# Kernel tuning notes

Hardware: AMD Instinct MI355X
Metric: run time of the kernel (lower is better)

## Reference

```python
import jax, jax.numpy as jnp
import numpy as np

B, S, D, H = 4, 2048, 1024, 16
DK = D // H
SCALE = 1.0 / np.float32(np.sqrt(DK))


def setup_inputs() -> dict:
    key = jax.random.key(0)
    ks = jax.random.split(key, 11)
    w = lambda k: (jax.random.normal(k, (D, D), jnp.float32) * 0.02)
    b = lambda k: (jax.random.normal(k, (D,), jnp.float32) * 0.02)
    return {
        "Q": jax.random.normal(ks[0], (B, S, D), jnp.float32),
        "K": jax.random.normal(ks[1], (B, S, D), jnp.float32),
        "V": jax.random.normal(ks[2], (B, S, D), jnp.float32),
        "Wq": w(ks[3]), "bq": b(ks[4]),
        "Wk": w(ks[5]), "bk": b(ks[6]),
        "Wv": w(ks[7]), "bv": b(ks[8]),
        "Wo": w(ks[9]), "bo": b(ks[10]),
        # causal mask, broadcast over batch and heads: [1,1,S,S]
        "mask": jnp.tril(jnp.ones((1, 1, S, S), dtype=bool)),
    }


def reference(Q, K, V, Wq, bq, Wk, bk, Wv, bv, Wo, bo, mask):
    def proj(x, W, bias):
        # [B,S,D] -> [B,H,S,DK]
        return (x @ W + bias).reshape(B, S, H, DK).transpose(0, 2, 1, 3)

    q = proj(Q, Wq, bq)
    k = proj(K, Wk, bk)
    v = proj(V, Wv, bv)
    scores = jnp.einsum("bhqd,bhkd->bhqk", q, k) * SCALE  # [B,H,S,S]
    scores = jnp.where(mask, scores, jnp.float32(-1e9))
    attn = jax.nn.softmax(scores, axis=-1)
    out = jnp.einsum("bhqk,bhkd->bhqd", attn, v)  # [B,H,S,DK]
    out = out.transpose(0, 2, 1, 3).reshape(B, S, D)
    return out @ Wo + bo
```

## Files before the change

### kernel.cpp

```cpp
#include <hip/hip_runtime.h>
#include <hip/hip_bf16.h>
#include <stdint.h>

#define BB 4
#define SS 2048
#define DD 1024
#define HH 16
#define DKK 64
#define MM (BB * SS)

typedef __hip_bfloat16 bf16;
typedef __attribute__((ext_vector_type(8))) short frag8;
typedef __attribute__((ext_vector_type(4))) float f32x4;

#define GLDS16(g, l)                                                        \
  __builtin_amdgcn_global_load_lds(                                         \
      (const __attribute__((address_space(1))) void*)(g),                   \
      (__attribute__((address_space(3))) void*)(l), 16, 0, 0)

#define MFMA __builtin_amdgcn_mfma_f32_16x16x32_bf16

__device__ __forceinline__ unsigned short f2bu(float f) {
  __hip_bfloat16 h = __float2bfloat16(f);
  return *reinterpret_cast<unsigned short*>(&h);
}

__global__ __launch_bounds__(1024) void wtrans_kernel(
    const float* __restrict__ W, unsigned short* __restrict__ Wt) {
  __shared__ float tile[32][33];
  const int tx = threadIdx.x, ty = threadIdx.y;
  const int n0 = blockIdx.x * 32, k0 = blockIdx.y * 32;
  tile[ty][tx] = W[(size_t)(k0 + ty) * DD + n0 + tx];
  __syncthreads();
  Wt[(size_t)(n0 + ty) * DD + k0 + tx] = f2bu(tile[tx][ty]);
}

template <int A_BF16, int OUT_MODE>
__global__ __launch_bounds__(256) void gemm_kernel(
    const void* __restrict__ Av, const unsigned short* __restrict__ Wt,
    const float* __restrict__ bias, void* __restrict__ outv, float oscale) {
  constexpr int K = DD;
  constexpr int ASTR = A_BF16 ? 32 : 40;
  __shared__ unsigned short Bs[128 * 32];
  __shared__ unsigned short As[128 * ASTR];
  const int tid = threadIdx.x;
  const int wave = tid >> 6, lane = tid & 63, quad = lane >> 4, l15 = lane & 15;
  const int wr = wave >> 1, wc = wave & 1;
  const int m0 = blockIdx.y * 128, n0 = blockIdx.x * 128;

  f32x4 acc[4][4] = {};

  for (int k0 = 0; k0 < K; k0 += 32) {
#pragma unroll
    for (int c = 0; c < 2; ++c) {
      const int row = c * 64 + wave * 16 + (lane >> 2);
      const int col8 = (lane & 3) * 8;
      const unsigned short* g = &Wt[(size_t)(n0 + row) * K + k0 + col8];
      unsigned off = __builtin_amdgcn_readfirstlane(
          (unsigned)(c * 4096 + wave * 1024));
      GLDS16(g, (char*)&Bs[0] + off);
    }
    if (A_BF16) {
      const unsigned short* A = (const unsigned short*)Av;
#pragma unroll
      for (int c = 0; c < 2; ++c) {
        const int row = c * 64 + wave * 16 + (lane >> 2);
        const int col8 = (lane & 3) * 8;
        const unsigned short* g = &A[(size_t)(m0 + row) * K + k0 + col8];
        unsigned off = __builtin_amdgcn_readfirstlane(
            (unsigned)(c * 4096 + wave * 1024));
        GLDS16(g, (char*)&As[0] + off);
      }
    } else {
      const float* A = (const float*)Av;
#pragma unroll
      for (int it = 0; it < 4; ++it) {
        const int row = tid / 8 + it * 32;
        const int col4 = (tid % 8) * 4;
        const float4 v = *(const float4*)&A[(size_t)(m0 + row) * K + k0 + col4];
        ushort4 u;
        u.x = f2bu(v.x); u.y = f2bu(v.y); u.z = f2bu(v.z); u.w = f2bu(v.w);
        *(ushort4*)&As[row * ASTR + col4] = u;
      }
    }
    __syncthreads();

    frag8 af[4], bfr[4];
#pragma unroll
    for (int mi = 0; mi < 4; ++mi)
      af[mi] = *(const frag8*)&As[(wr * 64 + mi * 16 + l15) * ASTR + quad * 8];
#pragma unroll
    for (int ni = 0; ni < 4; ++ni)
      bfr[ni] = *(const frag8*)&Bs[(wc * 64 + ni * 16 + l15) * 32 + quad * 8];
#pragma unroll
    for (int mi = 0; mi < 4; ++mi)
#pragma unroll
      for (int ni = 0; ni < 4; ++ni)
        acc[mi][ni] = MFMA(af[mi], bfr[ni], acc[mi][ni], 0, 0, 0);
    __syncthreads();
  }

#pragma unroll
  for (int mi = 0; mi < 4; ++mi) {
#pragma unroll
    for (int ni = 0; ni < 4; ++ni) {
#pragma unroll
      for (int r = 0; r < 4; ++r) {
        const int grow = m0 + wr * 64 + mi * 16 + quad * 4 + r;
        const int gcol = n0 + wc * 64 + ni * 16 + l15;
        const float val = (acc[mi][ni][r] + bias[gcol]) * oscale;
        if (OUT_MODE == 2) {
          ((float*)outv)[(size_t)grow * DD + gcol] = val;
        } else {
          const int b = grow / SS, s = grow % SS;
          const int h = gcol / DKK, dk = gcol % DKK;
          unsigned short* o = (unsigned short*)outv;
          if (OUT_MODE == 0)
            o[(((size_t)(b * HH + h)) * SS + s) * DKK + dk] = f2bu(val);
          else
            o[(((size_t)(b * HH + h)) * DKK + dk) * SS + s] = f2bu(val);
        }
      }
    }
  }
}

__global__ __launch_bounds__(256) void fattn_kernel(
    const unsigned short* __restrict__ q, const unsigned short* __restrict__ k,
    const unsigned short* __restrict__ vt, unsigned short* __restrict__ ctx) {
  __shared__ unsigned short Ks[2][64 * 64];
  __shared__ unsigned short Vs[2][64 * 64];
  __shared__ unsigned short P_lds[4][16][36];
  const int tid = threadIdx.x;
  const int wave = tid >> 6, lane = tid & 63, quad = lane >> 4, l15 = lane & 15;
  const int bh = blockIdx.x & 63;
  const int tp = blockIdx.x >> 6;
  const size_t qkb = (size_t)bh * SS * DKK;
  const size_t vtb = (size_t)bh * DKK * SS;
  const int b = bh / HH, h = bh % HH;

  frag8 ones;
#pragma unroll
  for (int s = 0; s < 8; ++s) ones[s] = (short)0x3F80;

  auto stage = [&](int buf, int jt) {
#pragma unroll
    for (int c = 0; c < 2; ++c) {
      const int row = wave * 16 + c * 8 + (lane >> 3);
      const int gc = ((lane & 7) ^ (row & 7)) * 8;
      const unsigned short* g = &k[qkb + (size_t)(jt * 64 + row) * DKK + gc];
      unsigned off = __builtin_amdgcn_readfirstlane(
          (unsigned)(buf * 8192 + (wave * 16 + c * 8) * 128));
      GLDS16(g, (char*)&Ks[0][0] + off);
    }
#pragma unroll
    for (int c = 0; c < 2; ++c) {
      const int row = wave * 16 + c * 8 + (lane >> 3);
      const int gc = ((lane & 7) ^ (row & 7)) * 8;
      const unsigned short* g = &vt[vtb + (size_t)row * SS + jt * 64 + gc];
      unsigned off = __builtin_amdgcn_readfirstlane(
          (unsigned)(buf * 8192 + (wave * 16 + c * 8) * 128));
      GLDS16(g, (char*)&Vs[0][0] + off);
    }
  };

  for (int half = 0; half < 2; ++half) {
    const int t = half ? (31 - tp) : tp;
    const int q0 = t * 64 + wave * 16;

    const frag8 aq0 =
        *(const frag8*)&q[qkb + (size_t)(q0 + l15) * DKK + quad * 8];
    const frag8 aq1 =
        *(const frag8*)&q[qkb + (size_t)(q0 + l15) * DKK + 32 + quad * 8];

    f32x4 oacc[4] = {};
    f32x4 lacc = {};

    const int nT = t + 1;
    stage(0, 0);
    __syncthreads();

    for (int jt = 0; jt < nT; ++jt) {
      const int p = jt & 1;
      if (jt + 1 < nT) stage(1 - p, jt + 1);
      const bool diag = (jt == t);

#pragma unroll
      for (int jsub = 0; jsub < 2; ++jsub) {
        f32x4 sc[2];
#pragma unroll
        for (int g = 0; g < 2; ++g) {
          const int row = jsub * 32 + g * 16 + l15;
          const frag8 kf0 =
              *(const frag8*)&Ks[p][row * 64 + ((quad ^ (l15 & 7)) * 8)];
          const frag8 kf1 =
              *(const frag8*)&Ks[p][row * 64 + (((4 + quad) ^ (l15 & 7)) * 8)];
          f32x4 z = {};
          z = MFMA(aq0, kf0, z, 0, 0, 0);
          sc[g] = MFMA(aq1, kf1, z, 0, 0, 0);
        }
        float p0[4], p1[4];
        if (diag) {
          const int jg = jt * 64 + jsub * 32;
#pragma unroll
          for (int r = 0; r < 4; ++r) {
            const int ig = q0 + quad * 4 + r;
            p0[r] = (jg + l15 <= ig) ? __expf(sc[0][r]) : 0.f;
            p1[r] = (jg + 16 + l15 <= ig) ? __expf(sc[1][r]) : 0.f;
          }
        } else {
#pragma unroll
          for (int r = 0; r < 4; ++r) {
            p0[r] = __expf(sc[0][r]);
            p1[r] = __expf(sc[1][r]);
          }
        }
#pragma unroll
        for (int r = 0; r < 4; ++r) {
          P_lds[wave][quad * 4 + r][l15] = f2bu(p0[r]);
          P_lds[wave][quad * 4 + r][16 + l15] = f2bu(p1[r]);
        }
        const frag8 pa = *(const frag8*)&P_lds[wave][l15][quad * 8];
#pragma unroll
        for (int c = 0; c < 4; ++c) {
          const int vrow = c * 16 + l15;
          const int chunk = ((jsub * 4 + quad) ^ (l15 & 7));
          const frag8 vf = *(const frag8*)&Vs[p][vrow * 64 + chunk * 8];
          oacc[c] = MFMA(pa, vf, oacc[c], 0, 0, 0);
        }
        lacc = MFMA(pa, ones, lacc, 0, 0, 0);
      }
      __syncthreads();
    }

#pragma unroll
    for (int r = 0; r < 4; ++r) {
      const float inv = 1.f / lacc[r];
      const int ig = q0 + quad * 4 + r;
#pragma unroll
      for (int c = 0; c < 4; ++c)
        ctx[((size_t)(b * SS + ig)) * DD + h * DKK + c * 16 + l15] =
            f2bu(oacc[c][r] * inv);
    }
  }
}

extern "C" void kernel_launch(void* const* d_in, const int* in_sizes, int n_in,
                              void* d_out, int out_size, void* d_ws,
                              size_t ws_size, hipStream_t stream) {
  const float* Q = (const float*)d_in[0];
  const float* K = (const float*)d_in[1];
  const float* V = (const float*)d_in[2];
  const float* Wq = (const float*)d_in[3];
  const float* bq = (const float*)d_in[4];
  const float* Wk = (const float*)d_in[5];
  const float* bk = (const float*)d_in[6];
  const float* Wv = (const float*)d_in[7];
  const float* bv = (const float*)d_in[8];
  const float* Wo = (const float*)d_in[9];
  const float* bo = (const float*)d_in[10];

  const size_t NE = (size_t)MM * DD;
  unsigned short* ctx = (unsigned short*)d_ws;
  unsigned short* qp = ctx + NE;
  unsigned short* kp = qp + NE;
  unsigned short* vtp = kp + NE;
  unsigned short* Wqt = ctx;
  unsigned short* Wkt = ctx + 1048576;
  unsigned short* Wvt = ctx + 2097152;
  unsigned short* Wot = qp;

  const dim3 tb(32, 32), tg(32, 32);
  const dim3 gg(DD / 128, MM / 128);

  wtrans_kernel<<<tg, tb, 0, stream>>>(Wq, Wqt);
  wtrans_kernel<<<tg, tb, 0, stream>>>(Wk, Wkt);
  wtrans_kernel<<<tg, tb, 0, stream>>>(Wv, Wvt);

  gemm_kernel<0, 0><<<gg, 256, 0, stream>>>((const void*)Q, Wqt, bq, qp,
                                            0.125f);
  gemm_kernel<0, 0><<<gg, 256, 0, stream>>>((const void*)K, Wkt, bk, kp, 1.f);
  gemm_kernel<0, 1><<<gg, 256, 0, stream>>>((const void*)V, Wvt, bv, vtp, 1.f);

  fattn_kernel<<<dim3(BB * HH * 16), 256, 0, stream>>>(qp, kp, vtp, ctx);

  wtrans_kernel<<<tg, tb, 0, stream>>>(Wo, Wot);
  gemm_kernel<1, 2><<<gg, 256, 0, stream>>>((const void*)ctx, Wot, bo,
                                            (void*)d_out, 1.f);
}
```

Before: 399.1 us.

## Double GEMM K-tile to 64 with XOR-swizzled LDS and batch weight transposes

Raises the GEMM K step from 32 to 64, so each iteration does two MFMA sub-steps per barrier pair. Shared tiles now use an XOR swizzle on 16-byte chunks instead of padding, to avoid LDS bank conflicts on the fragment reads. The weight-transpose kernel moves to 64x64 tiles with vectorized loads and packed bf16 stores, and the three Q/K/V transposes run as one launch. This cuts barrier and launch overhead, at the cost of twice the LDS per block, which may lower occupancy.

```diff
diff --git a/kernel.cpp b/kernel.cpp
--- a/kernel.cpp
+++ b/kernel.cpp
@@ -25,14 +25,33 @@
   return *reinterpret_cast<unsigned short*>(&h);
 }
 
-__global__ __launch_bounds__(1024) void wtrans_kernel(
-    const float* __restrict__ W, unsigned short* __restrict__ Wt) {
-  __shared__ float tile[32][33];
-  const int tx = threadIdx.x, ty = threadIdx.y;
-  const int n0 = blockIdx.x * 32, k0 = blockIdx.y * 32;
-  tile[ty][tx] = W[(size_t)(k0 + ty) * DD + n0 + tx];
+struct WtArgs {
+  const float* s[3];
+  unsigned short* d[3];
+};
+__global__ __launch_bounds__(256) void wtrans_kernel(WtArgs a) {
+  const float* __restrict__ W = a.s[blockIdx.z];
+  unsigned short* __restrict__ Wt = a.d[blockIdx.z];
+  __shared__ float t[64][68];
+  const int n0 = blockIdx.x * 64, k0 = blockIdx.y * 64;
+  const int tid = threadIdx.x;
+#pragma unroll
+  for (int it = 0; it < 4; ++it) {
+    const int kk = it * 16 + (tid >> 4);
+    const int nn = (tid & 15) * 4;
+    const float4 v = *(const float4*)&W[(size_t)(k0 + kk) * DD + n0 + nn];
+    *(float4*)&t[kk][nn] = v;
+  }
   __syncthreads();
-  Wt[(size_t)(n0 + ty) * DD + k0 + tx] = f2bu(tile[tx][ty]);
+#pragma unroll
+  for (int it = 0; it < 2; ++it) {
+    const int n = it * 32 + (tid >> 3);
+    const int c = tid & 7;
+    frag8 pk;
+#pragma unroll
+    for (int j = 0; j < 8; ++j) pk[j] = (short)f2bu(t[c * 8 + j][n]);
+    *(frag8*)&Wt[(size_t)(n0 + n) * DD + k0 + c * 8] = pk;
+  }
 }
 
 template <int A_BF16, int OUT_MODE>
@@ -40,9 +59,8 @@
     const void* __restrict__ Av, const unsigned short* __restrict__ Wt,
     const float* __restrict__ bias, void* __restrict__ outv, float oscale) {
   constexpr int K = DD;
-  constexpr int ASTR = A_BF16 ? 32 : 40;
-  __shared__ unsigned short Bs[128 * 32];
-  __shared__ unsigned short As[128 * ASTR];
+  __shared__ unsigned short Bs[128 * 64];
+  __shared__ unsigned short As[128 * 64];
   const int tid = threadIdx.x;
   const int wave = tid >> 6, lane = tid & 63, quad = lane >> 4, l15 = lane & 15;
   const int wr = wave >> 1, wc = wave & 1;
@@ -50,53 +68,63 @@
 
   f32x4 acc[4][4] = {};
 
-  for (int k0 = 0; k0 < K; k0 += 32) {
-#pragma unroll
-    for (int c = 0; c < 2; ++c) {
-      const int row = c * 64 + wave * 16 + (lane >> 2);
-      const int col8 = (lane & 3) * 8;
-      const unsigned short* g = &Wt[(size_t)(n0 + row) * K + k0 + col8];
+  for (int k0 = 0; k0 < K; k0 += 64) {
+#pragma unroll
+    for (int c = 0; c < 4; ++c) {
+      const int row = c * 32 + wave * 8 + (lane >> 3);
+      const int gc = ((lane & 7) ^ (row & 7)) * 8;
+      const unsigned short* g = &Wt[(size_t)(n0 + row) * K + k0 + gc];
       unsigned off = __builtin_amdgcn_readfirstlane(
-          (unsigned)(c * 4096 + wave * 1024));
+          (unsigned)((c * 32 + wave * 8) * 128));
       GLDS16(g, (char*)&Bs[0] + off);
     }
     if (A_BF16) {
       const unsigned short* A = (const unsigned short*)Av;
 #pragma unroll
-      for (int c = 0; c < 2; ++c) {
-        const int row = c * 64 + wave * 16 + (lane >> 2);
-        const int col8 = (lane & 3) * 8;
-        const unsigned short* g = &A[(size_t)(m0 + row) * K + k0 + col8];
+      for (int c = 0; c < 4; ++c) {
+        const int row = c * 32 + wave * 8 + (lane >> 3);
+        const int gc = ((lane & 7) ^ (row & 7)) * 8;
+        const unsigned short* g = &A[(size_t)(m0 + row) * K + k0 + gc];
         unsigned off = __builtin_amdgcn_readfirstlane(
-            (unsigned)(c * 4096 + wave * 1024));
+            (unsigned)((c * 32 + wave * 8) * 128));
         GLDS16(g, (char*)&As[0] + off);
       }
     } else {
       const float* A = (const float*)Av;
 #pragma unroll
       for (int it = 0; it < 4; ++it) {
-        const int row = tid / 8 + it * 32;
-        const int col4 = (tid % 8) * 4;
-        const float4 v = *(const float4*)&A[(size_t)(m0 + row) * K + k0 + col4];
-        ushort4 u;
-        u.x = f2bu(v.x); u.y = f2bu(v.y); u.z = f2bu(v.z); u.w = f2bu(v.w);
-        *(ushort4*)&As[row * ASTR + col4] = u;
+        const int row = it * 32 + (tid >> 3);
+        const int c = tid & 7;
+        const float4 v0 = *(const float4*)&A[(size_t)(m0 + row) * K + k0 + c * 8];
+        const float4 v1 =
+            *(const float4*)&A[(size_t)(m0 + row) * K + k0 + c * 8 + 4];
+        frag8 pk;
+        pk[0] = (short)f2bu(v0.x); pk[1] = (short)f2bu(v0.y);
+        pk[2] = (short)f2bu(v0.z); pk[3] = (short)f2bu(v0.w);
+        pk[4] = (short)f2bu(v1.x); pk[5] = (short)f2bu(v1.y);
+        pk[6] = (short)f2bu(v1.z); pk[7] = (short)f2bu(v1.w);
+        *(frag8*)&As[row * 64 + ((c ^ (row & 7)) * 8)] = pk;
       }
     }
     __syncthreads();
 
-    frag8 af[4], bfr[4];
-#pragma unroll
-    for (int mi = 0; mi < 4; ++mi)
-      af[mi] = *(const frag8*)&As[(wr * 64 + mi * 16 + l15) * ASTR + quad * 8];
-#pragma unroll
-    for (int ni = 0; ni < 4; ++ni)
-      bfr[ni] = *(const frag8*)&Bs[(wc * 64 + ni * 16 + l15) * 32 + quad * 8];
-#pragma unroll
-    for (int mi = 0; mi < 4; ++mi)
+#pragma unroll
+    for (int s = 0; s < 2; ++s) {
+      frag8 af[4], bfr[4];
+#pragma unroll
+      for (int mi = 0; mi < 4; ++mi)
+        af[mi] = *(const frag8*)
+            &As[(wr * 64 + mi * 16 + l15) * 64 + (((s * 4 + quad) ^ (l15 & 7)) * 8)];
 #pragma unroll
       for (int ni = 0; ni < 4; ++ni)
-        acc[mi][ni] = MFMA(af[mi], bfr[ni], acc[mi][ni], 0, 0, 0);
+        bfr[ni] = *(const frag8*)
+            &Bs[(wc * 64 + ni * 16 + l15) * 64 + (((s * 4 + quad) ^ (l15 & 7)) * 8)];
+#pragma unroll
+      for (int mi = 0; mi < 4; ++mi)
+#pragma unroll
+        for (int ni = 0; ni < 4; ++ni)
+          acc[mi][ni] = MFMA(af[mi], bfr[ni], acc[mi][ni], 0, 0, 0);
+    }
     __syncthreads();
   }
 
@@ -270,12 +298,12 @@
   unsigned short* Wvt = ctx + 2097152;
   unsigned short* Wot = qp;
 
-  const dim3 tb(32, 32), tg(32, 32);
   const dim3 gg(DD / 128, MM / 128);
 
-  wtrans_kernel<<<tg, tb, 0, stream>>>(Wq, Wqt);
-  wtrans_kernel<<<tg, tb, 0, stream>>>(Wk, Wkt);
-  wtrans_kernel<<<tg, tb, 0, stream>>>(Wv, Wvt);
+  WtArgs wa1;
+  wa1.s[0] = Wq; wa1.s[1] = Wk; wa1.s[2] = Wv;
+  wa1.d[0] = Wqt; wa1.d[1] = Wkt; wa1.d[2] = Wvt;
+  wtrans_kernel<<<dim3(16, 16, 3), 256, 0, stream>>>(wa1);
 
   gemm_kernel<0, 0><<<gg, 256, 0, stream>>>((const void*)Q, Wqt, bq, qp,
                                             0.125f);
@@ -284,7 +312,12 @@
 
   fattn_kernel<<<dim3(BB * HH * 16), 256, 0, stream>>>(qp, kp, vtp, ctx);
 
-  wtrans_kernel<<<tg, tb, 0, stream>>>(Wo, Wot);
+  WtArgs wa2;
+  wa2.s[0] = Wo; wa2.d[0] = Wot;
+  wa2.s[1] = Wo; wa2.d[1] = Wot;
+  wa2.s[2] = Wo; wa2.d[2] = Wot;
+  wtrans_kernel<<<dim3(16, 16, 1), 256, 0, stream>>>(wa2);
+
   gemm_kernel<1, 2><<<gg, 256, 0, stream>>>((const void*)ctx, Wot, bo,
                                             (void*)d_out, 1.f);
 }
```

Result: faster. 376.2 us (-5.7%).
